# Optimization experiments

Measured on AMD Instinct MI355X. Metric: run time of the kernel, lower is better.

## Reference

```python
import jax, jax.numpy as jnp
import numpy as np

NUM_ITER = 3
NUM_SLOTS = 8
INPUT_SIZE = 256
SLOT_SIZE = 256
MLP_HIDDEN = 512
HEADS = 4
EPSILON = 1e-8
LN_EPS = 1e-5


def _ln(x, g, b):
    m = jnp.mean(x, axis=-1, keepdims=True)
    v = jnp.mean((x - m) ** 2, axis=-1, keepdims=True)
    return (x - m) * jax.lax.rsqrt(v + LN_EPS) * g + b


def setup_inputs() -> dict:
    key = jax.random.key(0)
    ks = jax.random.split(key, 16)
    B, Nkv, Nq = 64, 1024, NUM_SLOTS
    S, D, Hm = SLOT_SIZE, INPUT_SIZE, MLP_HIDDEN
    def w(k, shape, fan_in):
        return jax.random.normal(k, shape, jnp.float32) * (fan_in ** -0.5)
    return {
        "inputs": jax.random.normal(ks[0], (B, Nkv, D), jnp.float32),
        "slots": jax.random.normal(ks[1], (B, Nq, S), jnp.float32),
        "ln_in_g": jnp.ones((D,), jnp.float32), "ln_in_b": jnp.zeros((D,), jnp.float32),
        "ln_sl_g": jnp.ones((S,), jnp.float32), "ln_sl_b": jnp.zeros((S,), jnp.float32),
        "ln_mlp_g": jnp.ones((S,), jnp.float32), "ln_mlp_b": jnp.zeros((S,), jnp.float32),
        "Wq": w(ks[2], (S, S), S),
        "Wk": w(ks[3], (D, S), D),
        "Wv": w(ks[4], (D, S), D),
        "gru_w_ih": w(ks[5], (3 * S, S), S),
        "gru_w_hh": w(ks[6], (3 * S, S), S),
        "gru_b_ih": jnp.zeros((3 * S,), jnp.float32),
        "gru_b_hh": jnp.zeros((3 * S,), jnp.float32),
        "mlp_w1": w(ks[7], (S, Hm), S),
        "mlp_b1": jnp.zeros((Hm,), jnp.float32),
        "mlp_w2": w(ks[8], (Hm, S), Hm),
        "mlp_b2": jnp.zeros((S,), jnp.float32),
    }


def reference(inputs, slots, ln_in_g, ln_in_b, ln_sl_g, ln_sl_b, ln_mlp_g, ln_mlp_b,
              Wq, Wk, Wv, gru_w_ih, gru_w_hh, gru_b_ih, gru_b_hh,
              mlp_w1, mlp_b1, mlp_w2, mlp_b2):
    B, Nkv, _ = inputs.shape
    _, Nq, S = slots.shape
    H = HEADS
    hd = S // H

    x = _ln(inputs, ln_in_g, ln_in_b)
    k = (x @ Wk).reshape(B, Nkv, H, hd).transpose(0, 2, 1, 3)  # [B,H,Nkv,hd]
    v = (x @ Wv).reshape(B, Nkv, H, hd).transpose(0, 2, 1, 3)  # [B,H,Nkv,hd]
    k = k * (hd ** -0.5)

    attn_vis = None
    for _ in range(NUM_ITER):
        slots_prev = slots
        s = _ln(slots, ln_sl_g, ln_sl_b)
        q = (s @ Wq).reshape(B, Nq, H, hd).transpose(0, 2, 1, 3)  # [B,H,Nq,hd]
        # logits [B,H,Nkv,Nq]
        logits = jnp.einsum('bhnd,bhqd->bhnq', k, q)
        # softmax over (heads * slots) jointly, per kv token
        flat = logits.transpose(0, 2, 1, 3).reshape(B, Nkv, H * Nq)
        attn = jax.nn.softmax(flat, axis=-1).reshape(B, Nkv, H, Nq).transpose(0, 2, 1, 3)
        attn_vis = attn.sum(axis=1).swapaxes(1, 2)  # [B,Nq,Nkv]
        attn = attn + EPSILON
        attn = attn / jnp.sum(attn, axis=-2, keepdims=True)  # normalize over Nkv
        updates = jnp.einsum('bhnq,bhnd->bqhd', attn, v).reshape(B, Nq, S)

        # GRU cell (torch gate order: r, z, n)
        xg = updates.reshape(-1, S) @ gru_w_ih.T + gru_b_ih
        hprev = slots_prev.reshape(-1, S)
        hg = hprev @ gru_w_hh.T + gru_b_hh
        xr, xz, xn = jnp.split(xg, 3, axis=-1)
        hr, hz, hn = jnp.split(hg, 3, axis=-1)
        r = jax.nn.sigmoid(xr + hr)
        z = jax.nn.sigmoid(xz + hz)
        n = jnp.tanh(xn + r * hn)
        h = (1.0 - z) * n + z * hprev
        slots = h.reshape(B, Nq, S)

        m = _ln(slots, ln_mlp_g, ln_mlp_b)
        slots = slots + (jax.nn.relu(m @ mlp_w1 + mlp_b1) @ mlp_w2 + mlp_b2)

    return slots, jax.lax.stop_gradient(attn_vis)
```

## Files before the change

kernel.cpp:

```cpp
#include <hip/hip_runtime.h>
#include <hip/hip_bf16.h>
#include <math.h>

#define EPS_  1e-8f
#define LNEPS 1e-5f

typedef __attribute__((ext_vector_type(8))) short   short8;
typedef __attribute__((ext_vector_type(8))) __bf16  bf16x8;
typedef __attribute__((ext_vector_type(4))) float   f32x4;
typedef unsigned short ushort_t;

__device__ __forceinline__ float bf2f(unsigned int u) { return __uint_as_float(u << 16); }
__device__ __forceinline__ unsigned short f2bf(float f) {
    unsigned int u = __float_as_uint(f);
    u += 0x7fff + ((u >> 16) & 1);
    return (unsigned short)(u >> 16);
}
__device__ __forceinline__ f32x4 mfma_bf16(short8 a, short8 b, f32x4 c) {
    union U { short8 s; bf16x8 b; };
    U ua, ub; ua.s = a; ub.s = b;
    return __builtin_amdgcn_mfma_f32_16x16x32_bf16(ua.b, ub.b, c, 0, 0, 0);
}
__device__ __forceinline__ float wred_sum(float v) {
#pragma unroll
    for (int off = 32; off > 0; off >>= 1) v += __shfl_xor(v, off);
    return v;
}

__global__ __launch_bounds__(256) void prepack_w_kernel(const float* __restrict__ Wk,
                                                        const float* __restrict__ Wv,
                                                        ushort_t* __restrict__ Wt) {
    int n = blockIdx.x;
    int k = threadIdx.x;
    float v = (n < 256) ? Wk[(size_t)k * 256 + n] * 0.125f : Wv[(size_t)k * 256 + (n - 256)];
    Wt[(size_t)n * 256 + k] = f2bf(v);
}

__global__ __launch_bounds__(256) void prepack_wtp_kernel(const ushort_t* __restrict__ Wt,
                                                          ushort_t* __restrict__ Wtp) {
    int bs = blockIdx.x;
    int wv = bs >> 3, s = bs & 7;
    int ni = threadIdx.x >> 6, l = threadIdx.x & 63;
    int n  = wv * 64 + ni * 16 + (l & 15);
    int k0 = s * 32 + (l >> 4) * 8;
    short8 v = *(const short8*)(Wt + (size_t)n * 256 + k0);
    *(short8*)(Wtp + ((size_t)bs * 4 + ni) * 512 + l * 8) = v;
}

__global__ __launch_bounds__(512) void prepack_slotw_kernel(const float* __restrict__ w_ih,
                                                            const float* __restrict__ w_hh,
                                                            const float* __restrict__ w1,
                                                            const float* __restrict__ w2,
                                                            const float* __restrict__ Wq,
                                                            ushort_t* __restrict__ wg,
                                                            ushort_t* __restrict__ w1p,
                                                            ushort_t* __restrict__ w2q,
                                                            ushort_t* __restrict__ Wqp) {
    int t = threadIdx.x, bid = blockIdx.x, sec = blockIdx.y;
    if (sec == 0) {
        if (bid < 256) {
            int k = bid, c = t & 255;
            const float* src = (t >> 8) ? w_hh : w_ih;
            size_t o = ((size_t)k * 512 + t) * 4;
            wg[o + 0] = f2bf(src[(size_t)(0 * 256 + c) * 256 + k]);
            wg[o + 1] = f2bf(src[(size_t)(1 * 256 + c) * 256 + k]);
            wg[o + 2] = f2bf(src[(size_t)(2 * 256 + c) * 256 + k]);
            wg[o + 3] = 0;
        }
    } else if (sec == 1) {
        if (bid < 64) {
            size_t o = ((size_t)bid * 512 + t) * 4;
#pragma unroll
            for (int i = 0; i < 4; i++) w1p[o + i] = f2bf(w1[(size_t)(bid * 4 + i) * 512 + t]);
        }
    } else if (sec == 2) {
        if (bid < 64) {
            int k4g = bid * 2 + (t >> 8), c = t & 255;
            size_t o = ((size_t)k4g * 256 + c) * 4;
#pragma unroll
            for (int i = 0; i < 4; i++) w2q[o + i] = f2bf(w2[(size_t)(k4g * 4 + i) * 256 + c]);
        }
    } else {
        if (bid < 32) {
            int k4g = bid * 2 + (t >> 8), c = t & 255;
            size_t o = ((size_t)k4g * 256 + c) * 4;
#pragma unroll
            for (int i = 0; i < 4; i++) Wqp[o + i] = f2bf(Wq[(size_t)(k4g * 4 + i) * 256 + c]);
        }
    }
}

__global__ __launch_bounds__(512, 4) void kvproj_mfma_kernel(const float* __restrict__ in,
                                                             const float* __restrict__ g,
                                                             const float* __restrict__ bb,
                                                             const ushort_t* __restrict__ Wtp,
                                                             ushort_t* __restrict__ kvout) {
    __shared__ __align__(16) ushort_t As[64 * 256];
    const int tid = threadIdx.x;
    const int wv = tid >> 6, l = tid & 63;
    const int kc = l >> 4, lr = l & 15;
    const int m0 = blockIdx.x * 64;

    float4 g4 = *(const float4*)(g + l * 4);
    float4 b4 = *(const float4*)(bb + l * 4);
    float4 xv[8];
#pragma unroll
    for (int i = 0; i < 8; i++)
        xv[i] = *(const float4*)(in + (size_t)(m0 + i * 8 + wv) * 256 + l * 4);
#pragma unroll
    for (int i = 0; i < 8; i++) {
        float s1 = xv[i].x + xv[i].y + xv[i].z + xv[i].w;
        float s2 = xv[i].x * xv[i].x + xv[i].y * xv[i].y + xv[i].z * xv[i].z + xv[i].w * xv[i].w;
        s1 = wred_sum(s1);
        s2 = wred_sum(s2);
        float m = s1 * (1.0f / 256.0f);
        float r = rsqrtf(s2 * (1.0f / 256.0f) - m * m + LNEPS);
        unsigned int p0 = f2bf((xv[i].x - m) * r * g4.x + b4.x);
        unsigned int p1 = f2bf((xv[i].y - m) * r * g4.y + b4.y);
        unsigned int p2 = f2bf((xv[i].z - m) * r * g4.z + b4.z);
        unsigned int p3 = f2bf((xv[i].w - m) * r * g4.w + b4.w);
        uint2 pk = {p0 | (p1 << 16), p2 | (p3 << 16)};
        int row = i * 8 + wv;
        *(uint2*)&As[row * 256 + (((l >> 1) ^ (row & 7)) * 8) + (l & 1) * 4] = pk;
    }
    __syncthreads();

    f32x4 zero = {0.f, 0.f, 0.f, 0.f};
    f32x4 acc[4][4];
#pragma unroll
    for (int i = 0; i < 4; i++)
#pragma unroll
        for (int jj = 0; jj < 4; jj++) acc[i][jj] = zero;

#pragma unroll
    for (int s = 0; s < 8; s++) {
        short8 bfr[4];
        const ushort_t* wpb = Wtp + ((size_t)(wv * 8 + s) * 4) * 512 + l * 8;
#pragma unroll
        for (int ni = 0; ni < 4; ni++) bfr[ni] = *(const short8*)(wpb + ni * 512);
        short8 af[4];
#pragma unroll
        for (int mi = 0; mi < 4; mi++) {
            int r2 = lr + mi * 16;
            int c = s * 4 + kc;
            af[mi] = *(const short8*)&As[r2 * 256 + ((c ^ (r2 & 7)) * 8)];
        }
#pragma unroll
        for (int mi = 0; mi < 4; mi++)
#pragma unroll
            for (int ni = 0; ni < 4; ni++)
                acc[mi][ni] = mfma_bf16(af[mi], bfr[ni], acc[mi][ni]);
    }
#pragma unroll
    for (int mi = 0; mi < 4; mi++)
#pragma unroll
        for (int ni = 0; ni < 4; ni++)
#pragma unroll
            for (int r = 0; r < 4; r++) {
                int rr2 = m0 + mi * 16 + kc * 4 + r;
                int col = wv * 64 + ni * 16 + lr;
                kvout[(size_t)rr2 * 512 + col] = f2bf(acc[mi][ni][r]);
            }
}

__global__ __launch_bounds__(256) void qproj_kernel(const float* __restrict__ slots,
                                                    const float* __restrict__ g,
                                                    const float* __restrict__ bvec,
                                                    const float* __restrict__ Wq,
                                                    float* __restrict__ qp) {
    int row = blockIdx.x;
    int tid = threadIdx.x;
    __shared__ float s_s[256];
    __shared__ float red[8];
    float x = slots[(size_t)row * 256 + tid];
    float s1 = wred_sum(x);
    float s2 = wred_sum(x * x);
    if ((tid & 63) == 0) { red[tid >> 6] = s1; red[4 + (tid >> 6)] = s2; }
    __syncthreads();
    float m  = (red[0] + red[1] + red[2] + red[3]) * (1.0f / 256.0f);
    float e2 = (red[4] + red[5] + red[6] + red[7]) * (1.0f / 256.0f);
    float rst = rsqrtf(e2 - m * m + LNEPS);
    s_s[tid] = (x - m) * rst * g[tid] + bvec[tid];
    __syncthreads();
    float acc = 0.f;
#pragma unroll 4
    for (int d = 0; d < 256; d++) acc += s_s[d] * Wq[(size_t)d * 256 + tid];
    int b = row >> 3, q = row & 7;
    qp[((size_t)(b * 4 + (tid >> 6)) * 8 + q) * 64 + (tid & 63)] = acc;
}

__global__ __launch_bounds__(256) void attn_fused_kernel(const ushort_t* __restrict__ kv,
                                                         const float* __restrict__ qp,
                                                         float* __restrict__ Upart,
                                                         float* __restrict__ Cpart,
                                                         float* __restrict__ vis,
                                                         int write_vis) {
    int b = blockIdx.y;
    int chunk = blockIdx.x;
    int tid = threadIdx.x;
    __shared__ __align__(16) ushort_t qfrag[16 * 512];
    __shared__ float att[128][32];
    __shared__ float ubuf[2][2048];
    __shared__ float cred[8][32];

    {
        const float* qb_ = qp + (size_t)b * 2048;
#pragma unroll
        for (int snt = 0; snt < 16; snt++) {
            int s = snt >> 1, nt = snt & 1;
#pragma unroll
            for (int rep = 0; rep < 2; rep++) {
                int idx = tid + rep * 256;
                int k  = s * 32 + ((idx >> 7) << 3) + (idx & 7);
                int hq = nt * 16 + ((idx >> 3) & 15);
                float v = ((k >> 6) == (hq >> 3))
                              ? qb_[(hq >> 3) * 512 + (hq & 7) * 64 + (k & 63)] : 0.f;
                qfrag[snt * 512 + idx] = f2bf(v);
            }
        }
    }
    __syncthreads();

    const int w = tid >> 6, l = tid & 63;
    const int lr = l & 15, kc8 = (l >> 4) * 8;

    short8 qb2[2][8];
#pragma unroll
    for (int s = 0; s < 8; s++) {
        qb2[0][s] = *(const short8*)&qfrag[(s * 2 + 0) * 512 + l * 8];
        qb2[1][s] = *(const short8*)&qfrag[(s * 2 + 1) * 512 + l * 8];
    }
    f32x4 zero = {0.f, 0.f, 0.f, 0.f};
#pragma unroll
    for (int mi_loc = 0; mi_loc < 2; mi_loc++) {
        int mi = w * 2 + mi_loc;
        f32x4 a0 = zero, a1 = zero;
        const ushort_t* abase = kv + (size_t)(b * 1024 + chunk * 128 + mi * 16 + lr) * 512 + kc8;
#pragma unroll
        for (int s = 0; s < 8; s++) {
            short8 af = *(const short8*)(abase + s * 32);
            a0 = mfma_bf16(af, qb2[0][s], a0);
            a1 = mfma_bf16(af, qb2[1][s], a1);
        }
        int row0 = mi * 16 + (l >> 4) * 4;
#pragma unroll
        for (int r = 0; r < 4; r++) {
            att[row0 + r][lr]      = a0[r];
            att[row0 + r][16 + lr] = a1[r];
        }
    }
    __syncthreads();

    {
        int token = tid >> 1, half = tid & 1;
        float v[16];
        float mx = -3.4e38f;
#pragma unroll
        for (int j = 0; j < 16; j++) { v[j] = att[token][half * 16 + j]; mx = fmaxf(mx, v[j]); }
        mx = fmaxf(mx, __shfl_xor(mx, 1));
        float sm = 0.f;
#pragma unroll
        for (int j = 0; j < 16; j++) { v[j] = __expf(v[j] - mx); sm += v[j]; }
        sm += __shfl_xor(sm, 1);
        float inv = 1.0f / sm;
#pragma unroll
        for (int j = 0; j < 16; j++) { v[j] *= inv; att[token][half * 16 + j] = v[j] + EPS_; }
        if (write_vis) {
#pragma unroll
            for (int q = 0; q < 8; q++) {
                float pv = v[q] + v[q + 8];
                float pf = pv + __shfl_xor(pv, 1);
                if (half == 0) vis[(size_t)(b * 8 + q) * 1024 + chunk * 128 + token] = pf;
            }
        }
    }
    __syncthreads();

    {
        int hq2 = tid & 31, grp = tid >> 5;
        float s = 0.f;
#pragma unroll
        for (int i = 0; i < 16; i++) s += att[grp * 16 + i][hq2];
        cred[grp][hq2] = s;
    }
    __syncthreads();
    if (tid < 32) {
        float s = 0.f;
#pragma unroll
        for (int g2 = 0; g2 < 8; g2++) s += cred[g2][tid];
        Cpart[(size_t)(b * 8 + chunk) * 32 + tid] = s;
    }

    const int h_u = l >> 4, d4 = l & 15;
    const int uo = h_u * 64 + d4 * 4;
    float U[8][4];
#pragma unroll
    for (int q = 0; q < 8; q++)
#pragma unroll
        for (int d = 0; d < 4; d++) U[q][d] = 0.f;
    const ushort_t* vbase = kv + (size_t)(b * 1024 + chunk * 128 + w * 32) * 512 + 256 + uo;
    for (int i = 0; i < 32; ++i) {
        uint2 vp = *(const uint2*)(vbase + (size_t)i * 512);
        float v0 = bf2f(vp.x & 0xffffu), v1 = bf2f(vp.x >> 16);
        float v2 = bf2f(vp.y & 0xffffu), v3 = bf2f(vp.y >> 16);
        const float* arow = &att[w * 32 + i][h_u * 8];
        float4 a01 = *(const float4*)(arow);
        float4 a23 = *(const float4*)(arow + 4);
        float aq[8] = {a01.x, a01.y, a01.z, a01.w, a23.x, a23.y, a23.z, a23.w};
#pragma unroll
        for (int q = 0; q < 8; q++) {
            U[q][0] += aq[q] * v0; U[q][1] += aq[q] * v1;
            U[q][2] += aq[q] * v2; U[q][3] += aq[q] * v3;
        }
    }
    if (w & 1) {
        float* dst = ubuf[w >> 1];
#pragma unroll
        for (int q = 0; q < 8; q++) {
            float4 uq = {U[q][0], U[q][1], U[q][2], U[q][3]};
            *(float4*)(dst + q * 256 + uo) = uq;
        }
    }
    __syncthreads();
    if (!(w & 1)) {
        const float* src = ubuf[w >> 1];
#pragma unroll
        for (int q = 0; q < 8; q++) {
            float4 uq = *(const float4*)(src + q * 256 + uo);
            U[q][0] += uq.x; U[q][1] += uq.y; U[q][2] += uq.z; U[q][3] += uq.w;
        }
    }
    __syncthreads();
    if (w == 2) {
        float* dst = ubuf[0];
#pragma unroll
        for (int q = 0; q < 8; q++) {
            float4 uq = {U[q][0], U[q][1], U[q][2], U[q][3]};
            *(float4*)(dst + q * 256 + uo) = uq;
        }
    }
    __syncthreads();
    if (w == 0) {
        const float* src = ubuf[0];
        float* up = Upart + (size_t)(b * 8 + chunk) * 2048 + uo;
#pragma unroll
        for (int q = 0; q < 8; q++) {
            float4 uq = *(const float4*)(src + q * 256 + uo);
            float4 o = {U[q][0] + uq.x, U[q][1] + uq.y, U[q][2] + uq.z, U[q][3] + uq.w};
            *(float4*)(up + q * 256) = o;
        }
    }
}

__global__ __launch_bounds__(1024) void slot_fused_kernel(const float* __restrict__ Upart,
                                                          const float* __restrict__ Cpart,
                                                          const float* __restrict__ slotsIn,
                                                          const ushort_t* __restrict__ wg,
                                                          const float* __restrict__ b_ih,
                                                          const float* __restrict__ b_hh,
                                                          const float* __restrict__ ln_mlp_g,
                                                          const float* __restrict__ ln_mlp_b,
                                                          const ushort_t* __restrict__ w1p,
                                                          const float* __restrict__ b1,
                                                          const ushort_t* __restrict__ w2q,
                                                          const float* __restrict__ b2,
                                                          const float* __restrict__ ln_sl_g,
                                                          const float* __restrict__ ln_sl_b,
                                                          const ushort_t* __restrict__ Wqp,
                                                          float* __restrict__ slotsOut,
                                                          float* __restrict__ qp,
                                                          int emit_qp) {
    __shared__ float U_s[2][256], H_s[2][256];
    __shared__ float rsum[2][2][256];
    __shared__ float gpart[2][12][256];
    __shared__ float SB_s[2][256], M_s[2][256];
    __shared__ float hid_s[2][512];
    __shared__ float mpart[2][2][512];
    __shared__ float ppart[4][2][256];
    __shared__ float redA[8], redB[8];
    const int t = threadIdx.x;
    const int kh = t >> 9, s9 = t & 511;
    const int rr = s9 >> 8, c = s9 & 255;
    const int lane = t & 63, wvi = t >> 6;
    const int r0 = blockIdx.x * 2;
    const int rg = r0 + rr, bb_ = rg >> 3, q = rg & 7;

    {
        float s = 0.f;
#pragma unroll
        for (int p2 = 0; p2 < 4; p2++)
            s += Upart[(size_t)(bb_ * 8 + kh * 4 + p2) * 2048 + q * 256 + c];
        rsum[kh][rr][c] = s;
    }
    __syncthreads();
    if (kh == 0) {
        int h = c >> 6;
        float C = 0.f;
#pragma unroll
        for (int p2 = 0; p2 < 8; p2++)
            C += Cpart[(size_t)(bb_ * 8 + p2) * 32 + h * 8 + q];
        U_s[rr][c] = (rsum[0][rr][c] + rsum[1][rr][c]) / C;
        H_s[rr][c] = slotsIn[(size_t)rg * 256 + c];
    }
    __syncthreads();

    {
        float ar0, az0, an0;
        if (kh == 0) {
            const float* bias = rr ? b_hh : b_ih;
            ar0 = bias[c]; az0 = bias[256 + c]; an0 = bias[512 + c];
        } else { ar0 = az0 = an0 = 0.f; }
        float ar1 = ar0, az1 = az0, an1 = an0;
        const float (*act)[256] = rr ? H_s : U_s;
        const ushort_t* wp = wg + (size_t)s9 * 4;
        for (int cc = 0; cc < 8; cc++) {
            uint2 wreg[16];
#pragma unroll
            for (int i = 0; i < 16; i++) {
                int k = kh * 128 + cc * 16 + i;
                wreg[i] = *(const uint2*)(wp + (size_t)k * 2048);
            }
#pragma unroll
            for (int i = 0; i < 16; i++) {
                int k = kh * 128 + cc * 16 + i;
                float w0  = bf2f(wreg[i].x & 0xffffu);
                float w1_ = bf2f(wreg[i].x >> 16);
                float w2_ = bf2f(wreg[i].y & 0xffffu);
                float a0 = act[0][k], a1 = act[1][k];
                ar0 += a0 * w0; az0 += a0 * w1_; an0 += a0 * w2_;
                ar1 += a1 * w0; az1 += a1 * w1_; an1 += a1 * w2_;
            }
        }
        gpart[kh][rr * 6 + 0][c] = ar0; gpart[kh][rr * 6 + 1][c] = ar1;
        gpart[kh][rr * 6 + 2][c] = az0; gpart[kh][rr * 6 + 3][c] = az1;
        gpart[kh][rr * 6 + 4][c] = an0; gpart[kh][rr * 6 + 5][c] = an1;
    }
    __syncthreads();

    float sb = 0.f;
    if (kh == 0) {
        float xr = gpart[0][0 + rr][c] + gpart[1][0 + rr][c];
        float xz = gpart[0][2 + rr][c] + gpart[1][2 + rr][c];
        float xn = gpart[0][4 + rr][c] + gpart[1][4 + rr][c];
        float hr = gpart[0][6 + rr][c] + gpart[1][6 + rr][c];
        float hz = gpart[0][8 + rr][c] + gpart[1][8 + rr][c];
        float hn = gpart[0][10 + rr][c] + gpart[1][10 + rr][c];
        float rg_ = 1.f / (1.f + __expf(-(xr + hr)));
        float z   = 1.f / (1.f + __expf(-(xz + hz)));
        float nn  = tanhf(xn + rg_ * hn);
        sb = (1.f - z) * nn + z * H_s[rr][c];
        SB_s[rr][c] = sb;
        float s1 = wred_sum(sb), s2 = wred_sum(sb * sb);
        if (lane == 0) { redA[wvi] = s1; redB[wvi] = s2; }
    }
    __syncthreads();
    if (kh == 0) {
        int base = rr * 4;
        float m  = (redA[base] + redA[base + 1] + redA[base + 2] + redA[base + 3]) * (1.f / 256.f);
        float e2 = (redB[base] + redB[base + 1] + redB[base + 2] + redB[base + 3]) * (1.f / 256.f);
        float rst = rsqrtf(e2 - m * m + LNEPS);
        M_s[rr][c] = (sb - m) * rst * ln_mlp_g[c] + ln_mlp_b[c];
    }
    __syncthreads();

    {
        float h10 = 0.f, h11 = 0.f;
        const ushort_t* wp = w1p + (size_t)s9 * 4;
        for (int cc = 0; cc < 2; cc++) {
            uint2 wreg[16];
#pragma unroll
            for (int i = 0; i < 16; i++) {
                int k4 = kh * 32 + cc * 16 + i;
                wreg[i] = *(const uint2*)(wp + (size_t)k4 * 2048);
            }
#pragma unroll
            for (int i = 0; i < 16; i++) {
                int k4 = kh * 32 + cc * 16 + i;
                float wA[4] = {bf2f(wreg[i].x & 0xffffu), bf2f(wreg[i].x >> 16),
                               bf2f(wreg[i].y & 0xffffu), bf2f(wreg[i].y >> 16)};
#pragma unroll
                for (int ii = 0; ii < 4; ii++) {
                    int k = k4 * 4 + ii;
                    h10 += M_s[0][k] * wA[ii];
                    h11 += M_s[1][k] * wA[ii];
                }
            }
        }
        mpart[kh][0][s9] = h10;
        mpart[kh][1][s9] = h11;
    }
    __syncthreads();
    if (kh == 0) {
        float bb1 = b1[s9];
        hid_s[0][s9] = fmaxf(mpart[0][0][s9] + mpart[1][0][s9] + bb1, 0.f);
        hid_s[1][s9] = fmaxf(mpart[0][1][s9] + mpart[1][1][s9] + bb1, 0.f);
    }
    __syncthreads();

    {
        int q2 = kh * 2 + rr;
        float p0 = 0.f, p1 = 0.f;
        const ushort_t* wp = w2q + (size_t)c * 4;
        for (int cc = 0; cc < 2; cc++) {
            uint2 wreg[16];
#pragma unroll
            for (int i = 0; i < 16; i++) {
                int k4g = q2 * 32 + cc * 16 + i;
                wreg[i] = *(const uint2*)(wp + (size_t)k4g * 1024);
            }
#pragma unroll
            for (int i = 0; i < 16; i++) {
                int k4g = q2 * 32 + cc * 16 + i;
                float wA[4] = {bf2f(wreg[i].x & 0xffffu), bf2f(wreg[i].x >> 16),
                               bf2f(wreg[i].y & 0xffffu), bf2f(wreg[i].y >> 16)};
#pragma unroll
                for (int ii = 0; ii < 4; ii++) {
                    int k = k4g * 4 + ii;
                    p0 += hid_s[0][k] * wA[ii];
                    p1 += hid_s[1][k] * wA[ii];
                }
            }
        }
        ppart[q2][0][c] = p0;
        ppart[q2][1][c] = p1;
    }
    __syncthreads();
    float outv = 0.f;
    if (kh == 0) {
        outv = ppart[0][rr][c] + ppart[1][rr][c] + ppart[2][rr][c] + ppart[3][rr][c]
             + b2[c] + SB_s[rr][c];
        slotsOut[(size_t)rg * 256 + c] = outv;
    }

    if (emit_qp) {
        __syncthreads();
        if (kh == 0) {
            float s1 = wred_sum(outv), s2 = wred_sum(outv * outv);
            if (lane == 0) { redA[wvi] = s1; redB[wvi] = s2; }
        }
        __syncthreads();
        if (kh == 0) {
            int base = rr * 4;
            float m  = (redA[base] + redA[base + 1] + redA[base + 2] + redA[base + 3]) * (1.f / 256.f);
            float e2 = (redB[base] + redB[base + 1] + redB[base + 2] + redB[base + 3]) * (1.f / 256.f);
            float rst = rsqrtf(e2 - m * m + LNEPS);
            M_s[rr][c] = (outv - m) * rst * ln_sl_g[c] + ln_sl_b[c];
        }
        __syncthreads();
        {
            int q2 = kh * 2 + rr;
            float p0 = 0.f, p1 = 0.f;
            const ushort_t* wp = Wqp + (size_t)c * 4;
            uint2 wreg[16];
#pragma unroll
            for (int i = 0; i < 16; i++) {
                int k4g = q2 * 16 + i;
                wreg[i] = *(const uint2*)(wp + (size_t)k4g * 1024);
            }
#pragma unroll
            for (int i = 0; i < 16; i++) {
                int k4g = q2 * 16 + i;
                float wA[4] = {bf2f(wreg[i].x & 0xffffu), bf2f(wreg[i].x >> 16),
                               bf2f(wreg[i].y & 0xffffu), bf2f(wreg[i].y >> 16)};
#pragma unroll
                for (int ii = 0; ii < 4; ii++) {
                    int k = k4g * 4 + ii;
                    p0 += M_s[0][k] * wA[ii];
                    p1 += M_s[1][k] * wA[ii];
                }
            }
            ppart[q2][0][c] = p0;
            ppart[q2][1][c] = p1;
        }
        __syncthreads();
        if (kh == 0) {
            float qv = ppart[0][rr][c] + ppart[1][rr][c] + ppart[2][rr][c] + ppart[3][rr][c];
            qp[(size_t)bb_ * 2048 + (c >> 6) * 512 + q * 64 + (c & 63)] = qv;
        }
    }
}

extern "C" void kernel_launch(void* const* d_in, const int* in_sizes, int n_in,
                              void* d_out, int out_size, void* d_ws, size_t ws_size,
                              hipStream_t stream) {
    const float* inputs   = (const float*)d_in[0];
    const float* slots0   = (const float*)d_in[1];
    const float* ln_in_g  = (const float*)d_in[2];
    const float* ln_in_b  = (const float*)d_in[3];
    const float* ln_sl_g  = (const float*)d_in[4];
    const float* ln_sl_b  = (const float*)d_in[5];
    const float* ln_mlp_g = (const float*)d_in[6];
    const float* ln_mlp_b = (const float*)d_in[7];
    const float* Wq       = (const float*)d_in[8];
    const float* Wk       = (const float*)d_in[9];
    const float* Wv       = (const float*)d_in[10];
    const float* w_ih     = (const float*)d_in[11];
    const float* w_hh     = (const float*)d_in[12];
    const float* b_ih     = (const float*)d_in[13];
    const float* b_hh     = (const float*)d_in[14];
    const float* w1       = (const float*)d_in[15];
    const float* b1       = (const float*)d_in[16];
    const float* w2       = (const float*)d_in[17];
    const float* b2       = (const float*)d_in[18];

    float* out_slots = (float*)d_out;
    float* out_vis   = (float*)d_out + 64 * 8 * 256;

    char* p = (char*)d_ws;
    auto carve = [&](size_t bytes) {
        void* r = (void*)p;
        p += (bytes + 255) & ~(size_t)255;
        return r;
    };
    ushort_t* kv   = (ushort_t*)carve((size_t)65536 * 512 * 2);
    ushort_t* Wt   = (ushort_t*)carve((size_t)512 * 256 * 2);
    ushort_t* Wtp  = (ushort_t*)carve((size_t)512 * 256 * 2);
    ushort_t* wg   = (ushort_t*)carve((size_t)256 * 512 * 4 * 2);
    ushort_t* w1p  = (ushort_t*)carve((size_t)64 * 512 * 4 * 2);
    ushort_t* w2q  = (ushort_t*)carve((size_t)128 * 256 * 4 * 2);
    ushort_t* Wqp  = (ushort_t*)carve((size_t)64 * 256 * 4 * 2);
    float* qp      = (float*)carve((size_t)64 * 2048 * 4);
    float* Upart   = (float*)carve((size_t)64 * 8 * 2048 * 4);
    float* Cpart   = (float*)carve((size_t)64 * 8 * 32 * 4);
    float* slotsA  = (float*)carve((size_t)512 * 256 * 4);

    prepack_w_kernel<<<512, 256, 0, stream>>>(Wk, Wv, Wt);
    prepack_wtp_kernel<<<64, 256, 0, stream>>>(Wt, Wtp);
    prepack_slotw_kernel<<<dim3(256, 4), 512, 0, stream>>>(w_ih, w_hh, w1, w2, Wq,
                                                           wg, w1p, w2q, Wqp);
    kvproj_mfma_kernel<<<1024, 512, 0, stream>>>(inputs, ln_in_g, ln_in_b, Wtp, kv);
    qproj_kernel<<<512, 256, 0, stream>>>(slots0, ln_sl_g, ln_sl_b, Wq, qp);

    for (int it = 0; it < 3; ++it) {
        attn_fused_kernel<<<dim3(8, 64), 256, 0, stream>>>(kv, qp, Upart, Cpart, out_vis,
                                                           (it == 2) ? 1 : 0);
        slot_fused_kernel<<<256, 1024, 0, stream>>>(
            Upart, Cpart, (it == 0) ? slots0 : slotsA,
            wg, b_ih, b_hh, ln_mlp_g, ln_mlp_b, w1p, b1, w2q, b2,
            ln_sl_g, ln_sl_b, Wqp,
            (it == 2) ? out_slots : slotsA, qp, (it < 2) ? 1 : 0);
    }
}
```

Before: 208.3 us.

## Split slot update into MFMA GEMM kernels and stage kvproj output through LDS

Replaces the monolithic scalar-FMA slot_fused kernel with a chain of kernels: an updates finalization step, MFMA bf16 GEMMs for the GRU input and hidden projections, a gate+LayerNorm kernel, MFMA GEMMs for both MLP layers, and qproj reused for the next query projection. Weights are prepacked into MFMA fragment layouts. The kvproj epilogue now stages results through padded shared memory so global stores are 16-byte coalesced. The aim is to use matrix cores for the per-iteration slot GEMMs and to improve kv store efficiency. In exchange it adds several launches per iteration and round-trips intermediates through global memory, and the small grids (8–48 blocks) leave most of the GPU idle.

```diff
diff --git a/kernel.cpp b/kernel.cpp
--- a/kernel.cpp
+++ b/kernel.cpp
@@ -39,54 +39,50 @@
 __global__ __launch_bounds__(256) void prepack_wtp_kernel(const ushort_t* __restrict__ Wt,
                                                           ushort_t* __restrict__ Wtp) {
     int bs = blockIdx.x;
-    int wv = bs >> 3, s = bs & 7;
     int ni = threadIdx.x >> 6, l = threadIdx.x & 63;
-    int n  = wv * 64 + ni * 16 + (l & 15);
+    int cg = bs >> 3, s = bs & 7;
+    int n  = cg * 64 + ni * 16 + (l & 15);
     int k0 = s * 32 + (l >> 4) * 8;
     short8 v = *(const short8*)(Wt + (size_t)n * 256 + k0);
     *(short8*)(Wtp + ((size_t)bs * 4 + ni) * 512 + l * 8) = v;
 }
 
-__global__ __launch_bounds__(512) void prepack_slotw_kernel(const float* __restrict__ w_ih,
+__global__ __launch_bounds__(256) void prepack_frags_kernel(const float* __restrict__ w_ih,
                                                             const float* __restrict__ w_hh,
                                                             const float* __restrict__ w1,
                                                             const float* __restrict__ w2,
-                                                            const float* __restrict__ Wq,
-                                                            ushort_t* __restrict__ wg,
-                                                            ushort_t* __restrict__ w1p,
-                                                            ushort_t* __restrict__ w2q,
-                                                            ushort_t* __restrict__ Wqp) {
-    int t = threadIdx.x, bid = blockIdx.x, sec = blockIdx.y;
-    if (sec == 0) {
-        if (bid < 256) {
-            int k = bid, c = t & 255;
-            const float* src = (t >> 8) ? w_hh : w_ih;
-            size_t o = ((size_t)k * 512 + t) * 4;
-            wg[o + 0] = f2bf(src[(size_t)(0 * 256 + c) * 256 + k]);
-            wg[o + 1] = f2bf(src[(size_t)(1 * 256 + c) * 256 + k]);
-            wg[o + 2] = f2bf(src[(size_t)(2 * 256 + c) * 256 + k]);
-            wg[o + 3] = 0;
-        }
-    } else if (sec == 1) {
-        if (bid < 64) {
-            size_t o = ((size_t)bid * 512 + t) * 4;
-#pragma unroll
-            for (int i = 0; i < 4; i++) w1p[o + i] = f2bf(w1[(size_t)(bid * 4 + i) * 512 + t]);
-        }
-    } else if (sec == 2) {
-        if (bid < 64) {
-            int k4g = bid * 2 + (t >> 8), c = t & 255;
-            size_t o = ((size_t)k4g * 256 + c) * 4;
-#pragma unroll
-            for (int i = 0; i < 4; i++) w2q[o + i] = f2bf(w2[(size_t)(k4g * 4 + i) * 256 + c]);
-        }
+                                                            ushort_t* __restrict__ ihfr,
+                                                            ushort_t* __restrict__ hhfr,
+                                                            ushort_t* __restrict__ w1fr,
+                                                            ushort_t* __restrict__ w2fr) {
+    int m = blockIdx.y, bs = blockIdx.x;
+    int ni = threadIdx.x >> 6, l = threadIdx.x & 63;
+    int nloc = ni * 16 + (l & 15);
+    int kb = (l >> 4) * 8;
+    short8 v;
+    if (m <= 1) {
+        if (bs >= 96) return;
+        int cg = bs >> 3, s = bs & 7;
+        const float* src = m ? w_hh : w_ih;
+        int n = cg * 64 + nloc, k0 = s * 32 + kb;
+#pragma unroll
+        for (int j = 0; j < 8; j++) v[j] = (short)f2bf(src[(size_t)n * 256 + k0 + j]);
+        ushort_t* dst = m ? hhfr : ihfr;
+        *(short8*)&dst[((size_t)bs * 4 + ni) * 512 + l * 8] = v;
+    } else if (m == 2) {
+        if (bs >= 64) return;
+        int cg = bs >> 3, s = bs & 7;
+        int n = cg * 64 + nloc, k0 = s * 32 + kb;
+#pragma unroll
+        for (int j = 0; j < 8; j++) v[j] = (short)f2bf(w1[(size_t)(k0 + j) * 512 + n]);
+        *(short8*)&w1fr[((size_t)bs * 4 + ni) * 512 + l * 8] = v;
     } else {
-        if (bid < 32) {
-            int k4g = bid * 2 + (t >> 8), c = t & 255;
-            size_t o = ((size_t)k4g * 256 + c) * 4;
-#pragma unroll
-            for (int i = 0; i < 4; i++) Wqp[o + i] = f2bf(Wq[(size_t)(k4g * 4 + i) * 256 + c]);
-        }
+        if (bs >= 64) return;
+        int cg = bs >> 4, s = bs & 15;
+        int n = cg * 64 + nloc, k0 = s * 32 + kb;
+#pragma unroll
+        for (int j = 0; j < 8; j++) v[j] = (short)f2bf(w2[(size_t)(k0 + j) * 256 + n]);
+        *(short8*)&w2fr[((size_t)bs * 4 + ni) * 512 + l * 8] = v;
     }
 }
 
@@ -95,7 +91,7 @@
                                                              const float* __restrict__ bb,
                                                              const ushort_t* __restrict__ Wtp,
                                                              ushort_t* __restrict__ kvout) {
-    __shared__ __align__(16) ushort_t As[64 * 256];
+    __shared__ __align__(16) ushort_t As[64 * 264];
     const int tid = threadIdx.x;
     const int wv = tid >> 6, l = tid & 63;
     const int kc = l >> 4, lr = l & 15;
@@ -151,16 +147,31 @@
             for (int ni = 0; ni < 4; ni++)
                 acc[mi][ni] = mfma_bf16(af[mi], bfr[ni], acc[mi][ni]);
     }
-#pragma unroll
-    for (int mi = 0; mi < 4; mi++)
-#pragma unroll
-        for (int ni = 0; ni < 4; ni++)
-#pragma unroll
-            for (int r = 0; r < 4; r++) {
-                int rr2 = m0 + mi * 16 + kc * 4 + r;
-                int col = wv * 64 + ni * 16 + lr;
-                kvout[(size_t)rr2 * 512 + col] = f2bf(acc[mi][ni][r]);
-            }
+    __syncthreads();
+#pragma unroll
+    for (int half = 0; half < 2; half++) {
+        if ((wv >> 2) == half) {
+            int cw = (wv & 3) * 64;
+#pragma unroll
+            for (int mi = 0; mi < 4; mi++)
+#pragma unroll
+                for (int ni = 0; ni < 4; ni++)
+#pragma unroll
+                    for (int r = 0; r < 4; r++)
+                        As[(mi * 16 + kc * 4 + r) * 264 + cw + ni * 16 + lr] =
+                            f2bf(acc[mi][ni][r]);
+        }
+        __syncthreads();
+        {
+            int row = tid >> 3, seg = tid & 7;
+            const ushort_t* srcp = &As[row * 264 + seg * 32];
+            ushort_t* dstp = kvout + (size_t)(m0 + row) * 512 + half * 256 + seg * 32;
+#pragma unroll
+            for (int j = 0; j < 4; j++)
+                *(uint4*)(dstp + j * 8) = *(const uint4*)(srcp + j * 8);
+        }
+        __syncthreads();
+    }
 }
 
 __global__ __launch_bounds__(256) void qproj_kernel(const float* __restrict__ slots,
@@ -352,232 +363,228 @@
     }
 }
 
-__global__ __launch_bounds__(1024) void slot_fused_kernel(const float* __restrict__ Upart,
-                                                          const float* __restrict__ Cpart,
-                                                          const float* __restrict__ slotsIn,
-                                                          const ushort_t* __restrict__ wg,
-                                                          const float* __restrict__ b_ih,
-                                                          const float* __restrict__ b_hh,
-                                                          const float* __restrict__ ln_mlp_g,
-                                                          const float* __restrict__ ln_mlp_b,
-                                                          const ushort_t* __restrict__ w1p,
-                                                          const float* __restrict__ b1,
-                                                          const ushort_t* __restrict__ w2q,
-                                                          const float* __restrict__ b2,
-                                                          const float* __restrict__ ln_sl_g,
-                                                          const float* __restrict__ ln_sl_b,
-                                                          const ushort_t* __restrict__ Wqp,
-                                                          float* __restrict__ slotsOut,
-                                                          float* __restrict__ qp,
-                                                          int emit_qp) {
-    __shared__ float U_s[2][256], H_s[2][256];
-    __shared__ float rsum[2][2][256];
-    __shared__ float gpart[2][12][256];
-    __shared__ float SB_s[2][256], M_s[2][256];
-    __shared__ float hid_s[2][512];
-    __shared__ float mpart[2][2][512];
-    __shared__ float ppart[4][2][256];
-    __shared__ float redA[8], redB[8];
+__global__ __launch_bounds__(256) void updates_final_kernel(const float* __restrict__ Upart,
+                                                            const float* __restrict__ Cpart,
+                                                            const float* __restrict__ slotsIn,
+                                                            ushort_t* __restrict__ U_bf,
+                                                            ushort_t* __restrict__ H_bf) {
+    int b = blockIdx.x, c = threadIdx.x, h = c >> 6;
+#pragma unroll
+    for (int q = 0; q < 8; q++) {
+        float C = 0.f, s = 0.f;
+#pragma unroll
+        for (int p = 0; p < 8; p++) {
+            C += Cpart[(size_t)(b * 8 + p) * 32 + h * 8 + q];
+            s += Upart[(size_t)(b * 8 + p) * 2048 + q * 256 + c];
+        }
+        int row = b * 8 + q;
+        U_bf[(size_t)row * 256 + c] = f2bf(s / C);
+        H_bf[(size_t)row * 256 + c] = f2bf(slotsIn[(size_t)row * 256 + c]);
+    }
+}
+
+__global__ __launch_bounds__(256) void gru_gemm_kernel(const ushort_t* __restrict__ U_bf,
+                                                       const ushort_t* __restrict__ H_bf,
+                                                       const ushort_t* __restrict__ ihfr,
+                                                       const ushort_t* __restrict__ hhfr,
+                                                       const float* __restrict__ b_ih,
+                                                       const float* __restrict__ b_hh,
+                                                       float* __restrict__ gg) {
+    __shared__ __align__(16) ushort_t As[64 * 256];
     const int t = threadIdx.x;
-    const int kh = t >> 9, s9 = t & 511;
-    const int rr = s9 >> 8, c = s9 & 255;
-    const int lane = t & 63, wvi = t >> 6;
-    const int r0 = blockIdx.x * 2;
-    const int rg = r0 + rr, bb_ = rg >> 3, q = rg & 7;
-
+    const int mtile = blockIdx.x, ntile = blockIdx.y, z = blockIdx.z;
+    const ushort_t* Abf = z ? H_bf : U_bf;
+    const ushort_t* fr  = z ? hhfr : ihfr;
+    const float* bias   = z ? b_hh : b_ih;
     {
-        float s = 0.f;
-#pragma unroll
-        for (int p2 = 0; p2 < 4; p2++)
-            s += Upart[(size_t)(bb_ * 8 + kh * 4 + p2) * 2048 + q * 256 + c];
-        rsum[kh][rr][c] = s;
-    }
-    __syncthreads();
-    if (kh == 0) {
-        int h = c >> 6;
-        float C = 0.f;
-#pragma unroll
-        for (int p2 = 0; p2 < 8; p2++)
-            C += Cpart[(size_t)(bb_ * 8 + p2) * 32 + h * 8 + q];
-        U_s[rr][c] = (rsum[0][rr][c] + rsum[1][rr][c]) / C;
-        H_s[rr][c] = slotsIn[(size_t)rg * 256 + c];
-    }
-    __syncthreads();
-
+        int row = t >> 2, seg = t & 3;
+        const ushort_t* src = Abf + (size_t)(mtile * 64 + row) * 256 + seg * 64;
+#pragma unroll
+        for (int i = 0; i < 8; i++) {
+            uint4 v = *(const uint4*)(src + i * 8);
+            int c = seg * 8 + i;
+            *(uint4*)&As[row * 256 + ((c ^ (row & 7)) * 8)] = v;
+        }
+    }
+    __syncthreads();
+    const int wv = t >> 6, l = t & 63, kc = l >> 4, lr = l & 15;
+    f32x4 zero = {0.f, 0.f, 0.f, 0.f};
+    f32x4 acc[4][4];
+#pragma unroll
+    for (int i = 0; i < 4; i++)
+#pragma unroll
+        for (int jj = 0; jj < 4; jj++) acc[i][jj] = zero;
+    const int cg = ntile * 4 + wv;
+#pragma unroll
+    for (int s = 0; s < 8; s++) {
+        short8 bfr[4];
+        const ushort_t* fp = fr + ((size_t)(cg * 8 + s) * 4) * 512 + l * 8;
+#pragma unroll
+        for (int ni = 0; ni < 4; ni++) bfr[ni] = *(const short8*)(fp + ni * 512);
+        short8 af[4];
+#pragma unroll
+        for (int mi = 0; mi < 4; mi++) {
+            int r2 = lr + mi * 16;
+            int c = s * 4 + kc;
+            af[mi] = *(const short8*)&As[r2 * 256 + ((c ^ (r2 & 7)) * 8)];
+        }
+#pragma unroll
+        for (int mi = 0; mi < 4; mi++)
+#pragma unroll
+            for (int ni = 0; ni < 4; ni++)
+                acc[mi][ni] = mfma_bf16(af[mi], bfr[ni], acc[mi][ni]);
+    }
+#pragma unroll
+    for (int mi = 0; mi < 4; mi++)
+#pragma unroll
+        for (int ni = 0; ni < 4; ni++)
+#pragma unroll
+            for (int r = 0; r < 4; r++) {
+                int rowg = mtile * 64 + mi * 16 + kc * 4 + r;
+                int ng = ntile * 256 + wv * 64 + ni * 16 + lr;
+                gg[(size_t)rowg * 1536 + z * 768 + ng] = acc[mi][ni][r] + bias[ng];
+            }
+}
+
+__global__ __launch_bounds__(256) void gate_ln_kernel(const float* __restrict__ gg,
+                                                      const float* __restrict__ slotsIn,
+                                                      const float* __restrict__ ln_g,
+                                                      const float* __restrict__ ln_b,
+                                                      float* __restrict__ SB,
+                                                      ushort_t* __restrict__ M_bf) {
+    int row = blockIdx.x, c = threadIdx.x;
+    __shared__ float red[8];
+    const float* gr = gg + (size_t)row * 1536;
+    float xr = gr[c], xz = gr[256 + c], xn = gr[512 + c];
+    float hr = gr[768 + c], hz = gr[1024 + c], hn = gr[1280 + c];
+    float hp = slotsIn[(size_t)row * 256 + c];
+    float rg = 1.f / (1.f + __expf(-(xr + hr)));
+    float z  = 1.f / (1.f + __expf(-(xz + hz)));
+    float nn = tanhf(xn + rg * hn);
+    float sb = (1.f - z) * nn + z * hp;
+    SB[(size_t)row * 256 + c] = sb;
+    float s1 = wred_sum(sb), s2 = wred_sum(sb * sb);
+    if ((c & 63) == 0) { red[c >> 6] = s1; red[4 + (c >> 6)] = s2; }
+    __syncthreads();
+    float m  = (red[0] + red[1] + red[2] + red[3]) * (1.0f / 256.0f);
+    float e2 = (red[4] + red[5] + red[6] + red[7]) * (1.0f / 256.0f);
+    float rst = rsqrtf(e2 - m * m + LNEPS);
+    M_bf[(size_t)row * 256 + c] = f2bf((sb - m) * rst * ln_g[c] + ln_b[c]);
+}
+
+__global__ __launch_bounds__(256) void mlp1_gemm_kernel(const ushort_t* __restrict__ M_bf,
+                                                        const ushort_t* __restrict__ w1fr,
+                                                        const float* __restrict__ b1,
+                                                        ushort_t* __restrict__ hid_bf) {
+    __shared__ __align__(16) ushort_t As[64 * 256];
+    const int t = threadIdx.x;
+    const int mtile = blockIdx.x, ntile = blockIdx.y;
     {
-        float ar0, az0, an0;
-        if (kh == 0) {
-            const float* bias = rr ? b_hh : b_ih;
-            ar0 = bias[c]; az0 = bias[256 + c]; an0 = bias[512 + c];
-        } else { ar0 = az0 = an0 = 0.f; }
-        float ar1 = ar0, az1 = az0, an1 = an0;
-        const float (*act)[256] = rr ? H_s : U_s;
-        const ushort_t* wp = wg + (size_t)s9 * 4;
-        for (int cc = 0; cc < 8; cc++) {
-            uint2 wreg[16];
-#pragma unroll
-            for (int i = 0; i < 16; i++) {
-                int k = kh * 128 + cc * 16 + i;
-                wreg[i] = *(const uint2*)(wp + (size_t)k * 2048);
+        int row = t >> 2, seg = t & 3;
+        const ushort_t* src = M_bf + (size_t)(mtile * 64 + row) * 256 + seg * 64;
+#pragma unroll
+        for (int i = 0; i < 8; i++) {
+            uint4 v = *(const uint4*)(src + i * 8);
+            int c = seg * 8 + i;
+            *(uint4*)&As[row * 256 + ((c ^ (row & 7)) * 8)] = v;
+        }
+    }
+    __syncthreads();
+    const int wv = t >> 6, l = t & 63, kc = l >> 4, lr = l & 15;
+    f32x4 zero = {0.f, 0.f, 0.f, 0.f};
+    f32x4 acc[4][4];
+#pragma unroll
+    for (int i = 0; i < 4; i++)
+#pragma unroll
+        for (int jj = 0; jj < 4; jj++) acc[i][jj] = zero;
+    const int cg = ntile * 4 + wv;
+#pragma unroll
+    for (int s = 0; s < 8; s++) {
+        short8 bfr[4];
+        const ushort_t* fp = w1fr + ((size_t)(cg * 8 + s) * 4) * 512 + l * 8;
+#pragma unroll
+        for (int ni = 0; ni < 4; ni++) bfr[ni] = *(const short8*)(fp + ni * 512);
+        short8 af[4];
+#pragma unroll
+        for (int mi = 0; mi < 4; mi++) {
+            int r2 = lr + mi * 16;
+            int c = s * 4 + kc;
+            af[mi] = *(const short8*)&As[r2 * 256 + ((c ^ (r2 & 7)) * 8)];
+        }
+#pragma unroll
+        for (int mi = 0; mi < 4; mi++)
+#pragma unroll
+            for (int ni = 0; ni < 4; ni++)
+                acc[mi][ni] = mfma_bf16(af[mi], bfr[ni], acc[mi][ni]);
+    }
+#pragma unroll
+    for (int mi = 0; mi < 4; mi++)
+#pragma unroll
+        for (int ni = 0; ni < 4; ni++)
+#pragma unroll
+            for (int r = 0; r < 4; r++) {
+                int rowg = mtile * 64 + mi * 16 + kc * 4 + r;
+                int ng = ntile * 256 + wv * 64 + ni * 16 + lr;
+                hid_bf[(size_t)rowg * 512 + ng] = f2bf(fmaxf(acc[mi][ni][r] + b1[ng], 0.f));
             }
-#pragma unroll
-            for (int i = 0; i < 16; i++) {
-                int k = kh * 128 + cc * 16 + i;
-                float w0  = bf2f(wreg[i].x & 0xffffu);
-                float w1_ = bf2f(wreg[i].x >> 16);
-                float w2_ = bf2f(wreg[i].y & 0xffffu);
-                float a0 = act[0][k], a1 = act[1][k];
-                ar0 += a0 * w0; az0 += a0 * w1_; an0 += a0 * w2_;
-                ar1 += a1 * w0; az1 += a1 * w1_; an1 += a1 * w2_;
+}
+
+__global__ __launch_bounds__(256) void mlp2_gemm_kernel(const ushort_t* __restrict__ hid_bf,
+                                                        const ushort_t* __restrict__ w2fr,
+                                                        const float* __restrict__ b2,
+                                                        const float* __restrict__ SB,
+                                                        float* __restrict__ outS) {
+    __shared__ __align__(16) ushort_t As[64 * 512];
+    const int t = threadIdx.x;
+    const int mtile = blockIdx.x;
+    {
+        int row = t >> 2, seg = t & 3;
+        const ushort_t* src = hid_bf + (size_t)(mtile * 64 + row) * 512 + seg * 128;
+#pragma unroll
+        for (int i = 0; i < 16; i++) {
+            uint4 v = *(const uint4*)(src + i * 8);
+            int c = seg * 16 + i;
+            *(uint4*)&As[row * 512 + ((c ^ (row & 7)) * 8)] = v;
+        }
+    }
+    __syncthreads();
+    const int wv = t >> 6, l = t & 63, kc = l >> 4, lr = l & 15;
+    f32x4 zero = {0.f, 0.f, 0.f, 0.f};
+    f32x4 acc[4][4];
+#pragma unroll
+    for (int i = 0; i < 4; i++)
+#pragma unroll
+        for (int jj = 0; jj < 4; jj++) acc[i][jj] = zero;
+#pragma unroll
+    for (int s = 0; s < 16; s++) {
+        short8 bfr[4];
+        const ushort_t* fp = w2fr + ((size_t)(wv * 16 + s) * 4) * 512 + l * 8;
+#pragma unroll
+        for (int ni = 0; ni < 4; ni++) bfr[ni] = *(const short8*)(fp + ni * 512);
+        short8 af[4];
+#pragma unroll
+        for (int mi = 0; mi < 4; mi++) {
+            int r2 = lr + mi * 16;
+            int c = s * 4 + kc;
+            af[mi] = *(const short8*)&As[r2 * 512 + ((c ^ (r2 & 7)) * 8)];
+        }
+#pragma unroll
+        for (int mi = 0; mi < 4; mi++)
+#pragma unroll
+            for (int ni = 0; ni < 4; ni++)
+                acc[mi][ni] = mfma_bf16(af[mi], bfr[ni], acc[mi][ni]);
+    }
+#pragma unroll
+    for (int mi = 0; mi < 4; mi++)
+#pragma unroll
+        for (int ni = 0; ni < 4; ni++)
+#pragma unroll
+            for (int r = 0; r < 4; r++) {
+                int rowg = mtile * 64 + mi * 16 + kc * 4 + r;
+                int col = wv * 64 + ni * 16 + lr;
+                outS[(size_t)rowg * 256 + col] =
+                    acc[mi][ni][r] + b2[col] + SB[(size_t)rowg * 256 + col];
             }
-        }
-        gpart[kh][rr * 6 + 0][c] = ar0; gpart[kh][rr * 6 + 1][c] = ar1;
-        gpart[kh][rr * 6 + 2][c] = az0; gpart[kh][rr * 6 + 3][c] = az1;
-        gpart[kh][rr * 6 + 4][c] = an0; gpart[kh][rr * 6 + 5][c] = an1;
-    }
-    __syncthreads();
-
-    float sb = 0.f;
-    if (kh == 0) {
-        float xr = gpart[0][0 + rr][c] + gpart[1][0 + rr][c];
-        float xz = gpart[0][2 + rr][c] + gpart[1][2 + rr][c];
-        float xn = gpart[0][4 + rr][c] + gpart[1][4 + rr][c];
-        float hr = gpart[0][6 + rr][c] + gpart[1][6 + rr][c];
-        float hz = gpart[0][8 + rr][c] + gpart[1][8 + rr][c];
-        float hn = gpart[0][10 + rr][c] + gpart[1][10 + rr][c];
-        float rg_ = 1.f / (1.f + __expf(-(xr + hr)));
-        float z   = 1.f / (1.f + __expf(-(xz + hz)));
-        float nn  = tanhf(xn + rg_ * hn);
-        sb = (1.f - z) * nn + z * H_s[rr][c];
-        SB_s[rr][c] = sb;
-        float s1 = wred_sum(sb), s2 = wred_sum(sb * sb);
-        if (lane == 0) { redA[wvi] = s1; redB[wvi] = s2; }
-    }
-    __syncthreads();
-    if (kh == 0) {
-        int base = rr * 4;
-        float m  = (redA[base] + redA[base + 1] + redA[base + 2] + redA[base + 3]) * (1.f / 256.f);
-        float e2 = (redB[base] + redB[base + 1] + redB[base + 2] + redB[base + 3]) * (1.f / 256.f);
-        float rst = rsqrtf(e2 - m * m + LNEPS);
-        M_s[rr][c] = (sb - m) * rst * ln_mlp_g[c] + ln_mlp_b[c];
-    }
-    __syncthreads();
-
-    {
-        float h10 = 0.f, h11 = 0.f;
-        const ushort_t* wp = w1p + (size_t)s9 * 4;
-        for (int cc = 0; cc < 2; cc++) {
-            uint2 wreg[16];
-#pragma unroll
-            for (int i = 0; i < 16; i++) {
-                int k4 = kh * 32 + cc * 16 + i;
-                wreg[i] = *(const uint2*)(wp + (size_t)k4 * 2048);
-            }
-#pragma unroll
-            for (int i = 0; i < 16; i++) {
-                int k4 = kh * 32 + cc * 16 + i;
-                float wA[4] = {bf2f(wreg[i].x & 0xffffu), bf2f(wreg[i].x >> 16),
-                               bf2f(wreg[i].y & 0xffffu), bf2f(wreg[i].y >> 16)};
-#pragma unroll
-                for (int ii = 0; ii < 4; ii++) {
-                    int k = k4 * 4 + ii;
-                    h10 += M_s[0][k] * wA[ii];
-                    h11 += M_s[1][k] * wA[ii];
-                }
-            }
-        }
-        mpart[kh][0][s9] = h10;
-        mpart[kh][1][s9] = h11;
-    }
-    __syncthreads();
-    if (kh == 0) {
-        float bb1 = b1[s9];
-        hid_s[0][s9] = fmaxf(mpart[0][0][s9] + mpart[1][0][s9] + bb1, 0.f);
-        hid_s[1][s9] = fmaxf(mpart[0][1][s9] + mpart[1][1][s9] + bb1, 0.f);
-    }
-    __syncthreads();
-
-    {
-        int q2 = kh * 2 + rr;
-        float p0 = 0.f, p1 = 0.f;
-        const ushort_t* wp = w2q + (size_t)c * 4;
-        for (int cc = 0; cc < 2; cc++) {
-            uint2 wreg[16];
-#pragma unroll
-            for (int i = 0; i < 16; i++) {
-                int k4g = q2 * 32 + cc * 16 + i;
-                wreg[i] = *(const uint2*)(wp + (size_t)k4g * 1024);
-            }
-#pragma unroll
-            for (int i = 0; i < 16; i++) {
-                int k4g = q2 * 32 + cc * 16 + i;
-                float wA[4] = {bf2f(wreg[i].x & 0xffffu), bf2f(wreg[i].x >> 16),
-                               bf2f(wreg[i].y & 0xffffu), bf2f(wreg[i].y >> 16)};
-#pragma unroll
-                for (int ii = 0; ii < 4; ii++) {
-                    int k = k4g * 4 + ii;
-                    p0 += hid_s[0][k] * wA[ii];
-                    p1 += hid_s[1][k] * wA[ii];
-                }
-            }
-        }
-        ppart[q2][0][c] = p0;
-        ppart[q2][1][c] = p1;
-    }
-    __syncthreads();
-    float outv = 0.f;
-    if (kh == 0) {
-        outv = ppart[0][rr][c] + ppart[1][rr][c] + ppart[2][rr][c] + ppart[3][rr][c]
-             + b2[c] + SB_s[rr][c];
-        slotsOut[(size_t)rg * 256 + c] = outv;
-    }
-
-    if (emit_qp) {
-        __syncthreads();
-        if (kh == 0) {
-            float s1 = wred_sum(outv), s2 = wred_sum(outv * outv);
-            if (lane == 0) { redA[wvi] = s1; redB[wvi] = s2; }
-        }
-        __syncthreads();
-        if (kh == 0) {
-            int base = rr * 4;
-            float m  = (redA[base] + redA[base + 1] + redA[base + 2] + redA[base + 3]) * (1.f / 256.f);
-            float e2 = (redB[base] + redB[base + 1] + redB[base + 2] + redB[base + 3]) * (1.f / 256.f);
-            float rst = rsqrtf(e2 - m * m + LNEPS);
-            M_s[rr][c] = (outv - m) * rst * ln_sl_g[c] + ln_sl_b[c];
-        }
-        __syncthreads();
-        {
-            int q2 = kh * 2 + rr;
-            float p0 = 0.f, p1 = 0.f;
-            const ushort_t* wp = Wqp + (size_t)c * 4;
-            uint2 wreg[16];
-#pragma unroll
-            for (int i = 0; i < 16; i++) {
-                int k4g = q2 * 16 + i;
-                wreg[i] = *(const uint2*)(wp + (size_t)k4g * 1024);
-            }
-#pragma unroll
-            for (int i = 0; i < 16; i++) {
-                int k4g = q2 * 16 + i;
-                float wA[4] = {bf2f(wreg[i].x & 0xffffu), bf2f(wreg[i].x >> 16),
-                               bf2f(wreg[i].y & 0xffffu), bf2f(wreg[i].y >> 16)};
-#pragma unroll
-                for (int ii = 0; ii < 4; ii++) {
-                    int k = k4g * 4 + ii;
-                    p0 += M_s[0][k] * wA[ii];
-                    p1 += M_s[1][k] * wA[ii];
-                }
-            }
-            ppart[q2][0][c] = p0;
-            ppart[q2][1][c] = p1;
-        }
-        __syncthreads();
-        if (kh == 0) {
-            float qv = ppart[0][rr][c] + ppart[1][rr][c] + ppart[2][rr][c] + ppart[3][rr][c];
-            qp[(size_t)bb_ * 2048 + (c >> 6) * 512 + q * 64 + (c & 63)] = qv;
-        }
-    }
 }
 
 extern "C" void kernel_launch(void* const* d_in, const int* in_sizes, int n_in,
@@ -612,32 +619,43 @@
         p += (bytes + 255) & ~(size_t)255;
         return r;
     };
-    ushort_t* kv   = (ushort_t*)carve((size_t)65536 * 512 * 2);
-    ushort_t* Wt   = (ushort_t*)carve((size_t)512 * 256 * 2);
-    ushort_t* Wtp  = (ushort_t*)carve((size_t)512 * 256 * 2);
-    ushort_t* wg   = (ushort_t*)carve((size_t)256 * 512 * 4 * 2);
-    ushort_t* w1p  = (ushort_t*)carve((size_t)64 * 512 * 4 * 2);
-    ushort_t* w2q  = (ushort_t*)carve((size_t)128 * 256 * 4 * 2);
-    ushort_t* Wqp  = (ushort_t*)carve((size_t)64 * 256 * 4 * 2);
-    float* qp      = (float*)carve((size_t)64 * 2048 * 4);
-    float* Upart   = (float*)carve((size_t)64 * 8 * 2048 * 4);
-    float* Cpart   = (float*)carve((size_t)64 * 8 * 32 * 4);
-    float* slotsA  = (float*)carve((size_t)512 * 256 * 4);
+    ushort_t* kv    = (ushort_t*)carve((size_t)65536 * 512 * 2);
+    ushort_t* Wt    = (ushort_t*)carve((size_t)512 * 256 * 2);
+    ushort_t* Wtp   = (ushort_t*)carve((size_t)512 * 256 * 2);
+    ushort_t* ihfr  = (ushort_t*)carve((size_t)768 * 256 * 2);
+    ushort_t* hhfr  = (ushort_t*)carve((size_t)768 * 256 * 2);
+    ushort_t* w1fr  = (ushort_t*)carve((size_t)512 * 256 * 2);
+    ushort_t* w2fr  = (ushort_t*)carve((size_t)256 * 512 * 2);
+    float* qp       = (float*)carve((size_t)64 * 2048 * 4);
+    float* Upart    = (float*)carve((size_t)64 * 8 * 2048 * 4);
+    float* Cpart    = (float*)carve((size_t)64 * 8 * 32 * 4);
+    float* gg       = (float*)carve((size_t)512 * 1536 * 4);
+    float* SB       = (float*)carve((size_t)512 * 256 * 4);
+    float* slotsA   = (float*)carve((size_t)512 * 256 * 4);
+    ushort_t* U_bf  = (ushort_t*)carve((size_t)512 * 256 * 2);
+    ushort_t* H_bf  = (ushort_t*)carve((size_t)512 * 256 * 2);
+    ushort_t* M_bf  = (ushort_t*)carve((size_t)512 * 256 * 2);
+    ushort_t* hid_bf = (ushort_t*)carve((size_t)512 * 512 * 2);
 
     prepack_w_kernel<<<512, 256, 0, stream>>>(Wk, Wv, Wt);
     prepack_wtp_kernel<<<64, 256, 0, stream>>>(Wt, Wtp);
-    prepack_slotw_kernel<<<dim3(256, 4), 512, 0, stream>>>(w_ih, w_hh, w1, w2, Wq,
-                                                           wg, w1p, w2q, Wqp);
+    prepack_frags_kernel<<<dim3(96, 4), 256, 0, stream>>>(w_ih, w_hh, w1, w2,
+                                                          ihfr, hhfr, w1fr, w2fr);
     kvproj_mfma_kernel<<<1024, 512, 0, stream>>>(inputs, ln_in_g, ln_in_b, Wtp, kv);
     qproj_kernel<<<512, 256, 0, stream>>>(slots0, ln_sl_g, ln_sl_b, Wq, qp);
 
     for (int it = 0; it < 3; ++it) {
+        const float* slotsIn = (it == 0) ? slots0 : slotsA;
+        float* slotsOut = (it == 2) ? out_slots : slotsA;
         attn_fused_kernel<<<dim3(8, 64), 256, 0, stream>>>(kv, qp, Upart, Cpart, out_vis,
                                                            (it == 2) ? 1 : 0);
-        slot_fused_kernel<<<256, 1024, 0, stream>>>(
-            Upart, Cpart, (it == 0) ? slots0 : slotsA,
-            wg, b_ih, b_hh, ln_mlp_g, ln_mlp_b, w1p, b1, w2q, b2,
-            ln_sl_g, ln_sl_b, Wqp,
-            (it == 2) ? out_slots : slotsA, qp, (it < 2) ? 1 : 0);
-    }
-}
+        updates_final_kernel<<<64, 256, 0, stream>>>(Upart, Cpart, slotsIn, U_bf, H_bf);
+        gru_gemm_kernel<<<dim3(8, 3, 2), 256, 0, stream>>>(U_bf, H_bf, ihfr, hhfr,
+                                                           b_ih, b_hh, gg);
+        gate_ln_kernel<<<512, 256, 0, stream>>>(gg, slotsIn, ln_mlp_g, ln_mlp_b, SB, M_bf);
+        mlp1_gemm_kernel<<<dim3(8, 2), 256, 0, stream>>>(M_bf, w1fr, b1, hid_bf);
+        mlp2_gemm_kernel<<<8, 256, 0, stream>>>(hid_bf, w2fr, b2, SB, slotsOut);
+        if (it < 2)
+            qproj_kernel<<<512, 256, 0, stream>>>(slotsA, ln_sl_g, ln_sl_b, Wq, qp);
+    }
+}
```

New measurement: 301.1 us. 1.45x slower.
